# Performance work log

Measured on AMD Instinct MI355X. Metric: run time of the kernel, lower is better.

Reference implementation:

```python
import jax, jax.numpy as jnp
import numpy as np

B, S, I, H = 64, 1024, 256, 256

def setup_inputs() -> dict:
    key = jax.random.key(0)
    k1, k2, k3 = jax.random.split(key, 3)
    x = jax.random.normal(k1, (B, S, I), dtype=jnp.float32)
    W = jax.random.normal(k2, (4 * H, H + I), dtype=jnp.float32) * (1.0 / np.sqrt(H + I))
    b = jax.random.normal(k3, (4 * H,), dtype=jnp.float32) * 0.01
    return {"x": x, "W": W, "b": b}

def reference(x, W, b):
    batch, seq_len, input_size = x.shape
    hidden = W.shape[1] - input_size
    # torch concat order is (hidden, x): first H columns of W act on h, rest on x
    W_h = W[:, :hidden]          # [4H, H]
    W_x = W[:, hidden:]          # [4H, I]
    # precompute input projections for all timesteps: [B, S, 4H]
    x_proj = jnp.einsum('bsi,gi->bsg', x, W_x) + b

    h0 = jnp.zeros((batch, hidden), dtype=x.dtype)
    c0 = jnp.zeros((batch, hidden), dtype=x.dtype)

    def step(carry, xp_t):
        h, c = carry
        gates = h @ W_h.T + xp_t                     # [B, 4H]
        f, i, g, o = jnp.split(gates, 4, axis=1)     # chunk order: forget, input, convert, output
        f = jax.nn.sigmoid(f)
        i = jax.nn.sigmoid(i)
        g = jnp.tanh(g)
        o = jax.nn.sigmoid(o)
        c_new = f * c + i * g
        h_new = o * jnp.tanh(c_new)
        return (h_new, c_new), h_new

    (h_fin, c_fin), outs = jax.lax.scan(step, (h0, c0), jnp.swapaxes(x_proj, 0, 1))
    outputs = jnp.swapaxes(outs, 0, 1)               # [B, S, H]
    return outputs, (h_fin, c_fin)
```

## Files before the change

### kernel.cpp

```cpp
#include <hip/hip_runtime.h>

typedef __attribute__((ext_vector_type(8))) short short8;
typedef __attribute__((ext_vector_type(4))) float f32x4;
typedef __attribute__((ext_vector_type(4))) unsigned u32x4;

__device__ __forceinline__ unsigned short f2bf(float f) {
  unsigned int u = __float_as_uint(f);
  u = (u + 0x7fffu + ((u >> 16) & 1u)) >> 16;
  return (unsigned short)u;
}

__device__ __forceinline__ void xp_store(float* p, float v) { *p = v; }
__device__ __forceinline__ void xp_store(unsigned short* p, float v) { *p = f2bf(v); }
__device__ __forceinline__ float xp_ld(const float* p) { return *p; }
__device__ __forceinline__ float xp_ld(const unsigned short* p) {
  return __uint_as_float(((unsigned int)*p) << 16);
}

__device__ __forceinline__ float quad_sum(float a) {
  float t1 = __int_as_float(
      __builtin_amdgcn_update_dpp(0, __float_as_int(a), 177, 0xf, 0xf, true));
  a += t1;
  float t2 = __int_as_float(
      __builtin_amdgcn_update_dpp(0, __float_as_int(a), 78, 0xf, 0xf, true));
  return a + t2;
}

__global__ void prep_wx(const float* __restrict__ W, unsigned int* __restrict__ Wx2) {
  int i = blockIdx.x * 256 + threadIdx.x;
  int g = i >> 7, kk = i & 127;
  float lo = W[(size_t)g * 512 + 256 + 2 * kk];
  float hi = W[(size_t)g * 512 + 256 + 2 * kk + 1];
  Wx2[i] = (unsigned int)f2bf(lo) | ((unsigned int)f2bf(hi) << 16);
}

__global__ void prep_wh(const float* __restrict__ W, unsigned int* __restrict__ Wh2) {
  int i = blockIdx.x * 256 + threadIdx.x;
  int r = i >> 7, kk = i & 127;
  float lo = W[(size_t)r * 512 + 2 * kk];
  float hi = W[(size_t)r * 512 + 2 * kk + 1];
  Wh2[i] = (unsigned int)f2bf(lo) | ((unsigned int)f2bf(hi) << 16);
}

template <typename XPT>
__global__ __launch_bounds__(256, 4) void gemm_xp(const float* __restrict__ x,
                                                  const unsigned int* __restrict__ Wx2,
                                                  const float* __restrict__ bias,
                                                  XPT* __restrict__ xp) {
  __shared__ unsigned short As[128][40];
  __shared__ unsigned short Bs[128][40];
  const int m0 = blockIdx.y * 128, n0 = blockIdx.x * 128;
  const int tid = threadIdx.x, lane = tid & 63, w = tid >> 6;
  const int wr = w >> 1, wc = w & 1;
  const int r16 = lane & 15, kq = lane >> 4;
  f32x4 acc[4][4];
#pragma unroll
  for (int m = 0; m < 4; m++)
#pragma unroll
    for (int n = 0; n < 4; n++)
#pragma unroll
      for (int j = 0; j < 4; j++) acc[m][n][j] = 0.f;

  for (int kb = 0; kb < 256; kb += 32) {
    __syncthreads();
#pragma unroll
    for (int i = 0; i < 4; i++) {
      int idx = tid + i * 256;
      int row = idx >> 3, c4 = idx & 7;
      float4 v = *(const float4*)(x + (size_t)(m0 + row) * 256 + kb + c4 * 4);
      ushort4 s;
      s.x = f2bf(v.x); s.y = f2bf(v.y); s.z = f2bf(v.z); s.w = f2bf(v.w);
      *(ushort4*)&As[row][c4 * 4] = s;
    }
#pragma unroll
    for (int i = 0; i < 2; i++) {
      int idx = tid + i * 256;
      int row = idx >> 2, c = idx & 3;
      uint4 v = *(const uint4*)(Wx2 + (size_t)(n0 + row) * 128 + (kb >> 1) + c * 4);
      *(uint4*)&Bs[row][c * 8] = v;
    }
    __syncthreads();
    short8 a[4], bb[4];
#pragma unroll
    for (int m = 0; m < 4; m++)
      a[m] = *(const short8*)&As[wr * 64 + m * 16 + r16][kq * 8];
#pragma unroll
    for (int n = 0; n < 4; n++)
      bb[n] = *(const short8*)&Bs[wc * 64 + n * 16 + r16][kq * 8];
#pragma unroll
    for (int m = 0; m < 4; m++)
#pragma unroll
      for (int n = 0; n < 4; n++)
        acc[m][n] = __builtin_amdgcn_mfma_f32_16x16x32_bf16(a[m], bb[n], acc[m][n], 0, 0, 0);
  }
#pragma unroll
  for (int n = 0; n < 4; n++) {
    int gn = n0 + wc * 64 + n * 16 + r16;
    float bi = bias[gn];
#pragma unroll
    for (int m = 0; m < 4; m++) {
      int gm = m0 + wr * 64 + m * 16 + kq * 4;
#pragma unroll
      for (int j = 0; j < 4; j++) {
        xp_store(&xp[(size_t)(gm + j) * 1024 + gn], acc[m][n][j] + bi);
      }
    }
  }
}

template <typename XPT>
__global__ __attribute__((amdgpu_flat_work_group_size(512, 512),
                          amdgpu_waves_per_eu(2, 2)))
void lstm_rec(const unsigned* __restrict__ Wh2,
              const XPT* __restrict__ xp,
              float* __restrict__ out) {
  __shared__ u32x4 wot[16 * 512];
  __shared__ unsigned hsh[2][4][136];

  const int tid = threadIdx.x;
  const int b = blockIdx.x;
  const int v = tid >> 2, p = tid & 3;
  const int brow0 = b << 10;

  const unsigned* fA_p = Wh2 + (size_t)(v) * 128 + (p << 5);
  const unsigned* iA_p = Wh2 + (size_t)(256 + v) * 128 + (p << 5);
  const unsigned* gA_p = Wh2 + (size_t)(512 + v) * 128 + (p << 5);
  const unsigned* oA_p = Wh2 + (size_t)(768 + v) * 128 + (p << 5);
  const unsigned* fB_p = Wh2 + (size_t)(128 + v) * 128 + (p << 5);
  const unsigned* iB_p = Wh2 + (size_t)(384 + v) * 128 + (p << 5);
  const unsigned* gB_p = Wh2 + (size_t)(640 + v) * 128 + (p << 5);
  const unsigned* oB_p = Wh2 + (size_t)(896 + v) * 128 + (p << 5);
  u32x4 fA0, fA1, fA2, fA3, fA4, fA5, fA6, fA7;
  u32x4 iA0, iA1, iA2, iA3, iA4, iA5, iA6, iA7;
  u32x4 gA0, gA1, gA2, gA3, gA4, gA5, gA6, gA7;
  u32x4 fB0, fB1, fB2, fB3, fB4, fB5, fB6, fB7;
  u32x4 iB0, iB1, iB2, iB3, iB4, iB5, iB6, iB7;
  u32x4 gB0, gB1, gB2, gB3, gB4, gB5, gB6, gB7;
#define LOADROW8(P, R0, R1, R2, R3, R4, R5, R6, R7)                   \
  asm volatile("global_load_dwordx4 %0, %8, off\n\t"                  \
               "global_load_dwordx4 %1, %8, off offset:16\n\t"        \
               "global_load_dwordx4 %2, %8, off offset:32\n\t"        \
               "global_load_dwordx4 %3, %8, off offset:48\n\t"        \
               "global_load_dwordx4 %4, %8, off offset:64\n\t"        \
               "global_load_dwordx4 %5, %8, off offset:80\n\t"        \
               "global_load_dwordx4 %6, %8, off offset:96\n\t"        \
               "global_load_dwordx4 %7, %8, off offset:112"           \
               : "=&v"(R0), "=&v"(R1), "=&v"(R2), "=&v"(R3),          \
                 "=&v"(R4), "=&v"(R5), "=&v"(R6), "=&v"(R7)           \
               : "v"(P)                                               \
               : "memory")
  LOADROW8(fA_p, fA0, fA1, fA2, fA3, fA4, fA5, fA6, fA7);
  LOADROW8(iA_p, iA0, iA1, iA2, iA3, iA4, iA5, iA6, iA7);
  LOADROW8(gA_p, gA0, gA1, gA2, gA3, gA4, gA5, gA6, gA7);
  LOADROW8(fB_p, fB0, fB1, fB2, fB3, fB4, fB5, fB6, fB7);
  LOADROW8(iB_p, iB0, iB1, iB2, iB3, iB4, iB5, iB6, iB7);
  LOADROW8(gB_p, gB0, gB1, gB2, gB3, gB4, gB5, gB6, gB7);
#undef LOADROW8
  asm volatile("s_waitcnt vmcnt(0)" ::: "memory");

#pragma unroll
  for (int E = 0; E < 8; E++) {
    wot[(E << 9) + tid] = *(const u32x4*)(oA_p + (E << 2));
    wot[((E + 8) << 9) + tid] = *(const u32x4*)(oB_p + (E << 2));
  }

  for (int i = tid; i < 2 * 4 * 136; i += 512) ((unsigned*)hsh)[i] = 0u;
  float c0 = 0.f, c1 = 0.f;
  float* outp = out + ((size_t)brow0 << 8);
  __syncthreads();

#define BAR() asm volatile("s_waitcnt lgkmcnt(0)\n\ts_barrier" ::: "memory")
#define DOT2(ACC, WD, HD) \
  asm("v_dot2_f32_bf16 %0, %1, %2, %0" : "+v"(ACC) : "v"(WD), "v"(HD))
#define DOTC(FA, IA, GA, FB, IB, GB, OA, OB, HJ)                    \
  {                                                                 \
    DOT2(aF0, FA[0], (HJ)[0]); DOT2(aF0, FA[1], (HJ)[1]);           \
    DOT2(aF0, FA[2], (HJ)[2]); DOT2(aF0, FA[3], (HJ)[3]);           \
    DOT2(aI0, IA[0], (HJ)[0]); DOT2(aI0, IA[1], (HJ)[1]);           \
    DOT2(aI0, IA[2], (HJ)[2]); DOT2(aI0, IA[3], (HJ)[3]);           \
    DOT2(aG0, GA[0], (HJ)[0]); DOT2(aG0, GA[1], (HJ)[1]);           \
    DOT2(aG0, GA[2], (HJ)[2]); DOT2(aG0, GA[3], (HJ)[3]);           \
    DOT2(aO0, (OA)[0], (HJ)[0]); DOT2(aO0, (OA)[1], (HJ)[1]);       \
    DOT2(aO0, (OA)[2], (HJ)[2]); DOT2(aO0, (OA)[3], (HJ)[3]);       \
    DOT2(aF1, FB[0], (HJ)[0]); DOT2(aF1, FB[1], (HJ)[1]);           \
    DOT2(aF1, FB[2], (HJ)[2]); DOT2(aF1, FB[3], (HJ)[3]);           \
    DOT2(aI1, IB[0], (HJ)[0]); DOT2(aI1, IB[1], (HJ)[1]);           \
    DOT2(aI1, IB[2], (HJ)[2]); DOT2(aI1, IB[3], (HJ)[3]);           \
    DOT2(aG1, GB[0], (HJ)[0]); DOT2(aG1, GB[1], (HJ)[1]);           \
    DOT2(aG1, GB[2], (HJ)[2]); DOT2(aG1, GB[3], (HJ)[3]);           \
    DOT2(aO1, (OB)[0], (HJ)[0]); DOT2(aO1, (OB)[1], (HJ)[1]);       \
    DOT2(aO1, (OB)[2], (HJ)[2]); DOT2(aO1, (OB)[3], (HJ)[3]);       \
  }
#define HJC(HRX, J) (*(const u32x4*)&hsh[HRX][p][(p << 5) + ((J) << 2)])

#define LSTM1(AF, AI, AG, AO, X0, X1, X2, X3, CC, HOUT)             \
  {                                                                 \
    float gf = AF + X0, gi = AI + X1, gg = AG + X2, go = AO + X3;   \
    float f = 1.f / (1.f + __expf(-gf));                            \
    float ii = 1.f / (1.f + __expf(-gi));                           \
    float eg = __expf(2.f * gg);                                    \
    float gtv = (eg - 1.f) / (eg + 1.f);                            \
    float o = 1.f / (1.f + __expf(-go));                            \
    CC = f * CC + ii * gtv;                                         \
    float ec = __expf(2.f * CC);                                    \
    float tc = (ec - 1.f) / (ec + 1.f);                             \
    HOUT = o * tc;                                                  \
  }

#define STEP(T, HR, HW)                                                                \
  {                                                                                    \
    const int t = (T);                                                                 \
          \
    const XPT* xr = xp + ((size_t)(brow0 + t) << 10);                                  \
    float xv0 = xp_ld(xr + v),        xv1 = xp_ld(xr + 256 + v);                       \
    float xv2 = xp_ld(xr + 512 + v),  xv3 = xp_ld(xr + 768 + v);                       \
    float xw0 = xp_ld(xr + 128 + v),  xw1 = xp_ld(xr + 384 + v);                       \
    float xw2 = xp_ld(xr + 640 + v),  xw3 = xp_ld(xr + 896 + v);                       \
                                                     \
    u32x4 hX = HJC(HR, 0), oAX = wot[(0 << 9) + tid], oBX = wot[(8 << 9) + tid];       \
    u32x4 hY = HJC(HR, 1), oAY = wot[(1 << 9) + tid], oBY = wot[(9 << 9) + tid];       \
    float aF0 = 0.f, aI0 = 0.f, aG0 = 0.f, aO0 = 0.f;                                  \
    float aF1 = 0.f, aI1 = 0.f, aG1 = 0.f, aO1 = 0.f;                                  \
    DOTC(fA0, iA0, gA0, fB0, iB0, gB0, oAX, oBX, hX)                                   \
    hX = HJC(HR, 2); oAX = wot[(2 << 9) + tid]; oBX = wot[(10 << 9) + tid];            \
    DOTC(fA1, iA1, gA1, fB1, iB1, gB1, oAY, oBY, hY)                                   \
    hY = HJC(HR, 3); oAY = wot[(3 << 9) + tid]; oBY = wot[(11 << 9) + tid];            \
    DOTC(fA2, iA2, gA2, fB2, iB2, gB2, oAX, oBX, hX)                                   \
    hX = HJC(HR, 4); oAX = wot[(4 << 9) + tid]; oBX = wot[(12 << 9) + tid];            \
    DOTC(fA3, iA3, gA3, fB3, iB3, gB3, oAY, oBY, hY)                                   \
    hY = HJC(HR, 5); oAY = wot[(5 << 9) + tid]; oBY = wot[(13 << 9) + tid];            \
    DOTC(fA4, iA4, gA4, fB4, iB4, gB4, oAX, oBX, hX)                                   \
    hX = HJC(HR, 6); oAX = wot[(6 << 9) + tid]; oBX = wot[(14 << 9) + tid];            \
    DOTC(fA5, iA5, gA5, fB5, iB5, gB5, oAY, oBY, hY)                                   \
    hY = HJC(HR, 7); oAY = wot[(7 << 9) + tid]; oBY = wot[(15 << 9) + tid];            \
    DOTC(fA6, iA6, gA6, fB6, iB6, gB6, oAX, oBX, hX)                                   \
    DOTC(fA7, iA7, gA7, fB7, iB7, gB7, oAY, oBY, hY)                                   \
                 \
    aF0 = quad_sum(aF0); aI0 = quad_sum(aI0); aG0 = quad_sum(aG0); aO0 = quad_sum(aO0);\
    aF1 = quad_sum(aF1); aI1 = quad_sum(aI1); aG1 = quad_sum(aG1); aO1 = quad_sum(aO1);\
    float h0v, h1v;                                                                    \
    LSTM1(aF0, aI0, aG0, aO0, xv0, xv1, xv2, xv3, c0, h0v)                             \
    LSTM1(aF1, aI1, aG1, aO1, xw0, xw1, xw2, xw3, c1, h1v)                             \
                   \
    ((unsigned short*)&hsh[HW][p][0])[v] = f2bf(h0v);                                  \
    ((unsigned short*)&hsh[HW][p][0])[v + 128] = f2bf(h1v);                            \
    if (p == 0) {                                                                      \
      __builtin_nontemporal_store(h0v, outp + ((size_t)t << 8) + v);                   \
      __builtin_nontemporal_store(h1v, outp + ((size_t)t << 8) + v + 128);             \
      if (t == 1023) {                                                                 \
        out[16777216 + b * 256 + v] = h0v;                                             \
        out[16777216 + b * 256 + v + 128] = h1v;                                       \
        out[16777216 + 16384 + b * 256 + v] = c0;                                      \
        out[16777216 + 16384 + b * 256 + v + 128] = c1;                                \
      }                                                                                \
    }                                                                                  \
           \
    BAR();                                                                             \
  }

  for (int t2 = 0; t2 < 1024; t2 += 2) {
    STEP(t2, 1, 0)
    STEP(t2 + 1, 0, 1)
  }
#undef STEP
#undef LSTM1
#undef HJC
#undef DOTC
#undef DOT2
#undef BAR
}

extern "C" void kernel_launch(void* const* d_in, const int* in_sizes, int n_in,
                              void* d_out, int out_size, void* d_ws, size_t ws_size,
                              hipStream_t stream) {
  (void)in_sizes; (void)n_in; (void)out_size;
  const float* x = (const float*)d_in[0];
  const float* W = (const float*)d_in[1];
  const float* bias = (const float*)d_in[2];
  float* out = (float*)d_out;
  char* ws = (char*)d_ws;

  unsigned int* Wx2 = (unsigned int*)ws;
  unsigned int* Wh2 = (unsigned int*)(ws + 524288);
  char* xpmem = ws + 1048576;

  const size_t need32 = 1048576 + (size_t)65536 * 1024 * 4;

  prep_wx<<<512, 256, 0, stream>>>(W, Wx2);
  prep_wh<<<512, 256, 0, stream>>>(W, Wh2);

  if (ws_size >= need32) {
    gemm_xp<float><<<dim3(8, 512), 256, 0, stream>>>(x, Wx2, bias, (float*)xpmem);
    lstm_rec<float><<<64, 512, 0, stream>>>(Wh2, (const float*)xpmem, out);
  } else {
    gemm_xp<unsigned short><<<dim3(8, 512), 256, 0, stream>>>(x, Wx2, bias,
                                                              (unsigned short*)xpmem);
    lstm_rec<unsigned short><<<64, 512, 0, stream>>>(Wh2, (const unsigned short*)xpmem, out);
  }
}
```

Baseline: 2.106 ms.

## Replace dot2 recurrent matvec with MFMA 16x16x32 bf16 using prepacked fragment layout

The per-step recurrent h@W_h^T product switches from v_dot2_f32_bf16 plus quad DPP reductions to MFMA 16x16x32 bf16 instructions. W_h is repacked into MFMA B-fragment order by a new prep kernel and mostly held in registers, with the remaining k-tiles in LDS. The hidden state is broadcast as the A operand, so only the first row of each 16-row MFMA tile is useful and most of that MFMA work is wasted. The aim is to shorten the per-step critical path and drop the cross-lane reductions, at the cost of MFMA latency and fewer lanes doing the gate math and stores.

```diff
diff --git a/kernel.cpp b/kernel.cpp
--- a/kernel.cpp
+++ b/kernel.cpp
@@ -15,15 +15,6 @@
 __device__ __forceinline__ float xp_ld(const float* p) { return *p; }
 __device__ __forceinline__ float xp_ld(const unsigned short* p) {
   return __uint_as_float(((unsigned int)*p) << 16);
-}
-
-__device__ __forceinline__ float quad_sum(float a) {
-  float t1 = __int_as_float(
-      __builtin_amdgcn_update_dpp(0, __float_as_int(a), 177, 0xf, 0xf, true));
-  a += t1;
-  float t2 = __int_as_float(
-      __builtin_amdgcn_update_dpp(0, __float_as_int(a), 78, 0xf, 0xf, true));
-  return a + t2;
 }
 
 __global__ void prep_wx(const float* __restrict__ W, unsigned int* __restrict__ Wx2) {
@@ -34,12 +25,15 @@
   Wx2[i] = (unsigned int)f2bf(lo) | ((unsigned int)f2bf(hi) << 16);
 }
 
-__global__ void prep_wh(const float* __restrict__ W, unsigned int* __restrict__ Wh2) {
+__global__ void prep_whB(const float* __restrict__ W, unsigned* __restrict__ WhB) {
   int i = blockIdx.x * 256 + threadIdx.x;
-  int r = i >> 7, kk = i & 127;
-  float lo = W[(size_t)r * 512 + 2 * kk];
-  float hi = W[(size_t)r * 512 + 2 * kk + 1];
-  Wh2[i] = (unsigned int)f2bf(lo) | ((unsigned int)f2bf(hi) << 16);
+  int f = i >> 8, lane = (i >> 2) & 63, jd = i & 3;
+  int w = f >> 6, n = (f >> 3) & 7, kt = f & 7;
+  int g = 256 * (n >> 1) + 32 * w + 16 * (n & 1) + (lane & 15);
+  int k = kt * 32 + ((lane >> 4) << 3) + 2 * jd;
+  float lo = W[(size_t)g * 512 + k];
+  float hi = W[(size_t)g * 512 + k + 1];
+  WhB[i] = (unsigned)f2bf(lo) | ((unsigned)f2bf(hi) << 16);
 }
 
 template <typename XPT>
@@ -111,88 +105,66 @@
 template <typename XPT>
 __global__ __attribute__((amdgpu_flat_work_group_size(512, 512),
                           amdgpu_waves_per_eu(2, 2)))
-void lstm_rec(const unsigned* __restrict__ Wh2,
+void lstm_rec(const unsigned* __restrict__ WhB,
               const XPT* __restrict__ xp,
               float* __restrict__ out) {
-  __shared__ u32x4 wot[16 * 512];
-  __shared__ unsigned hsh[2][4][136];
+  __shared__ u32x4 wotB[16 * 512];
+  __shared__ unsigned short hl[2][256];
 
   const int tid = threadIdx.x;
   const int b = blockIdx.x;
-  const int v = tid >> 2, p = tid & 3;
+  const int lane = tid & 63, w = tid >> 6;
+  const int c = lane & 15;
   const int brow0 = b << 10;
 
-  const unsigned* fA_p = Wh2 + (size_t)(v) * 128 + (p << 5);
-  const unsigned* iA_p = Wh2 + (size_t)(256 + v) * 128 + (p << 5);
-  const unsigned* gA_p = Wh2 + (size_t)(512 + v) * 128 + (p << 5);
-  const unsigned* oA_p = Wh2 + (size_t)(768 + v) * 128 + (p << 5);
-  const unsigned* fB_p = Wh2 + (size_t)(128 + v) * 128 + (p << 5);
-  const unsigned* iB_p = Wh2 + (size_t)(384 + v) * 128 + (p << 5);
-  const unsigned* gB_p = Wh2 + (size_t)(640 + v) * 128 + (p << 5);
-  const unsigned* oB_p = Wh2 + (size_t)(896 + v) * 128 + (p << 5);
-  u32x4 fA0, fA1, fA2, fA3, fA4, fA5, fA6, fA7;
-  u32x4 iA0, iA1, iA2, iA3, iA4, iA5, iA6, iA7;
-  u32x4 gA0, gA1, gA2, gA3, gA4, gA5, gA6, gA7;
-  u32x4 fB0, fB1, fB2, fB3, fB4, fB5, fB6, fB7;
-  u32x4 iB0, iB1, iB2, iB3, iB4, iB5, iB6, iB7;
-  u32x4 gB0, gB1, gB2, gB3, gB4, gB5, gB6, gB7;
-#define LOADROW8(P, R0, R1, R2, R3, R4, R5, R6, R7)                   \
-  asm volatile("global_load_dwordx4 %0, %8, off\n\t"                  \
-               "global_load_dwordx4 %1, %8, off offset:16\n\t"        \
-               "global_load_dwordx4 %2, %8, off offset:32\n\t"        \
-               "global_load_dwordx4 %3, %8, off offset:48\n\t"        \
-               "global_load_dwordx4 %4, %8, off offset:64\n\t"        \
-               "global_load_dwordx4 %5, %8, off offset:80\n\t"        \
-               "global_load_dwordx4 %6, %8, off offset:96\n\t"        \
-               "global_load_dwordx4 %7, %8, off offset:112"           \
-               : "=&v"(R0), "=&v"(R1), "=&v"(R2), "=&v"(R3),          \
-                 "=&v"(R4), "=&v"(R5), "=&v"(R6), "=&v"(R7)           \
-               : "v"(P)                                               \
-               : "memory")
-  LOADROW8(fA_p, fA0, fA1, fA2, fA3, fA4, fA5, fA6, fA7);
-  LOADROW8(iA_p, iA0, iA1, iA2, iA3, iA4, iA5, iA6, iA7);
-  LOADROW8(gA_p, gA0, gA1, gA2, gA3, gA4, gA5, gA6, gA7);
-  LOADROW8(fB_p, fB0, fB1, fB2, fB3, fB4, fB5, fB6, fB7);
-  LOADROW8(iB_p, iB0, iB1, iB2, iB3, iB4, iB5, iB6, iB7);
-  LOADROW8(gB_p, gB0, gB1, gB2, gB3, gB4, gB5, gB6, gB7);
-#undef LOADROW8
+  short8 B00, B01, B02, B03, B04, B05, B10, B11, B12, B13, B14, B15;
+  short8 B20, B21, B22, B23, B24, B25, B30, B31, B32, B33, B34, B35;
+  short8 B40, B41, B42, B43, B44, B45, B50, B51, B52, B53, B54, B55;
+  short8 B60, B61, B62, B63, B64, B65, B70, B71, B72, B73, B74, B75;
+#define LOADB4(P, R0, R1, R2, R3)                                     \
+  asm volatile("global_load_dwordx4 %0, %4, off\n\t"                  \
+               "global_load_dwordx4 %1, %4, off offset:1024\n\t"      \
+               "global_load_dwordx4 %2, %4, off offset:2048\n\t"      \
+               "global_load_dwordx4 %3, %4, off offset:3072"          \
+               : "=&v"(R0), "=&v"(R1), "=&v"(R2), "=&v"(R3)           \
+               : "v"(P) : "memory")
+#define LOADB2(P, R0, R1)                                             \
+  asm volatile("global_load_dwordx4 %0, %2, off\n\t"                  \
+               "global_load_dwordx4 %1, %2, off offset:1024"          \
+               : "=&v"(R0), "=&v"(R1) : "v"(P) : "memory")
+#define LOADN(N, RA, RB, RC, RD, RE, RF)                              \
+  {                                                                   \
+    const unsigned* bp = WhB + ((((w << 3) + N) << 11)) + (lane << 2);\
+    LOADB4(bp, RA, RB, RC, RD);                                       \
+    LOADB2(bp + 1024, RE, RF);                                        \
+  }
+  LOADN(0, B00, B01, B02, B03, B04, B05)
+  LOADN(1, B10, B11, B12, B13, B14, B15)
+  LOADN(2, B20, B21, B22, B23, B24, B25)
+  LOADN(3, B30, B31, B32, B33, B34, B35)
+  LOADN(4, B40, B41, B42, B43, B44, B45)
+  LOADN(5, B50, B51, B52, B53, B54, B55)
+  LOADN(6, B60, B61, B62, B63, B64, B65)
+  LOADN(7, B70, B71, B72, B73, B74, B75)
+#undef LOADN
+#undef LOADB4
+#undef LOADB2
   asm volatile("s_waitcnt vmcnt(0)" ::: "memory");
 
 #pragma unroll
-  for (int E = 0; E < 8; E++) {
-    wot[(E << 9) + tid] = *(const u32x4*)(oA_p + (E << 2));
-    wot[((E + 8) << 9) + tid] = *(const u32x4*)(oB_p + (E << 2));
-  }
-
-  for (int i = tid; i < 2 * 4 * 136; i += 512) ((unsigned*)hsh)[i] = 0u;
+  for (int s = 0; s < 16; s++) {
+    int n = s >> 1, kt = 6 + (s & 1);
+    wotB[(s << 9) + tid] =
+        *(const u32x4*)(WhB + ((((w << 3) + n) << 3) + kt) * 256 + (lane << 2));
+  }
+
+  if (tid < 256) { hl[0][tid] = 0; hl[1][tid] = 0; }
   float c0 = 0.f, c1 = 0.f;
   float* outp = out + ((size_t)brow0 << 8);
   __syncthreads();
 
 #define BAR() asm volatile("s_waitcnt lgkmcnt(0)\n\ts_barrier" ::: "memory")
-#define DOT2(ACC, WD, HD) \
-  asm("v_dot2_f32_bf16 %0, %1, %2, %0" : "+v"(ACC) : "v"(WD), "v"(HD))
-#define DOTC(FA, IA, GA, FB, IB, GB, OA, OB, HJ)                    \
-  {                                                                 \
-    DOT2(aF0, FA[0], (HJ)[0]); DOT2(aF0, FA[1], (HJ)[1]);           \
-    DOT2(aF0, FA[2], (HJ)[2]); DOT2(aF0, FA[3], (HJ)[3]);           \
-    DOT2(aI0, IA[0], (HJ)[0]); DOT2(aI0, IA[1], (HJ)[1]);           \
-    DOT2(aI0, IA[2], (HJ)[2]); DOT2(aI0, IA[3], (HJ)[3]);           \
-    DOT2(aG0, GA[0], (HJ)[0]); DOT2(aG0, GA[1], (HJ)[1]);           \
-    DOT2(aG0, GA[2], (HJ)[2]); DOT2(aG0, GA[3], (HJ)[3]);           \
-    DOT2(aO0, (OA)[0], (HJ)[0]); DOT2(aO0, (OA)[1], (HJ)[1]);       \
-    DOT2(aO0, (OA)[2], (HJ)[2]); DOT2(aO0, (OA)[3], (HJ)[3]);       \
-    DOT2(aF1, FB[0], (HJ)[0]); DOT2(aF1, FB[1], (HJ)[1]);           \
-    DOT2(aF1, FB[2], (HJ)[2]); DOT2(aF1, FB[3], (HJ)[3]);           \
-    DOT2(aI1, IB[0], (HJ)[0]); DOT2(aI1, IB[1], (HJ)[1]);           \
-    DOT2(aI1, IB[2], (HJ)[2]); DOT2(aI1, IB[3], (HJ)[3]);           \
-    DOT2(aG1, GB[0], (HJ)[0]); DOT2(aG1, GB[1], (HJ)[1]);           \
-    DOT2(aG1, GB[2], (HJ)[2]); DOT2(aG1, GB[3], (HJ)[3]);           \
-    DOT2(aO1, (OB)[0], (HJ)[0]); DOT2(aO1, (OB)[1], (HJ)[1]);       \
-    DOT2(aO1, (OB)[2], (HJ)[2]); DOT2(aO1, (OB)[3], (HJ)[3]);       \
-  }
-#define HJC(HRX, J) (*(const u32x4*)&hsh[HRX][p][(p << 5) + ((J) << 2)])
-
+#define MF(A, Bf, C) __builtin_amdgcn_mfma_f32_16x16x32_bf16(A, Bf, C, 0, 0, 0)
 #define LSTM1(AF, AI, AG, AO, X0, X1, X2, X3, CC, HOUT)             \
   {                                                                 \
     float gf = AF + X0, gi = AI + X1, gg = AG + X2, go = AO + X3;   \
@@ -207,54 +179,79 @@
     HOUT = o * tc;                                                  \
   }
 
-#define STEP(T, HR, HW)                                                                \
+#define STEP(T, RS, WS)                                                                \
   {                                                                                    \
     const int t = (T);                                                                 \
-          \
+             \
     const XPT* xr = xp + ((size_t)(brow0 + t) << 10);                                  \
-    float xv0 = xp_ld(xr + v),        xv1 = xp_ld(xr + 256 + v);                       \
-    float xv2 = xp_ld(xr + 512 + v),  xv3 = xp_ld(xr + 768 + v);                       \
-    float xw0 = xp_ld(xr + 128 + v),  xw1 = xp_ld(xr + 384 + v);                       \
-    float xw2 = xp_ld(xr + 640 + v),  xw3 = xp_ld(xr + 896 + v);                       \
-                                                     \
-    u32x4 hX = HJC(HR, 0), oAX = wot[(0 << 9) + tid], oBX = wot[(8 << 9) + tid];       \
-    u32x4 hY = HJC(HR, 1), oAY = wot[(1 << 9) + tid], oBY = wot[(9 << 9) + tid];       \
-    float aF0 = 0.f, aI0 = 0.f, aG0 = 0.f, aO0 = 0.f;                                  \
-    float aF1 = 0.f, aI1 = 0.f, aG1 = 0.f, aO1 = 0.f;                                  \
-    DOTC(fA0, iA0, gA0, fB0, iB0, gB0, oAX, oBX, hX)                                   \
-    hX = HJC(HR, 2); oAX = wot[(2 << 9) + tid]; oBX = wot[(10 << 9) + tid];            \
-    DOTC(fA1, iA1, gA1, fB1, iB1, gB1, oAY, oBY, hY)                                   \
-    hY = HJC(HR, 3); oAY = wot[(3 << 9) + tid]; oBY = wot[(11 << 9) + tid];            \
-    DOTC(fA2, iA2, gA2, fB2, iB2, gB2, oAX, oBX, hX)                                   \
-    hX = HJC(HR, 4); oAX = wot[(4 << 9) + tid]; oBX = wot[(12 << 9) + tid];            \
-    DOTC(fA3, iA3, gA3, fB3, iB3, gB3, oAY, oBY, hY)                                   \
-    hY = HJC(HR, 5); oAY = wot[(5 << 9) + tid]; oBY = wot[(13 << 9) + tid];            \
-    DOTC(fA4, iA4, gA4, fB4, iB4, gB4, oAX, oBX, hX)                                   \
-    hX = HJC(HR, 6); oAX = wot[(6 << 9) + tid]; oBX = wot[(14 << 9) + tid];            \
-    DOTC(fA5, iA5, gA5, fB5, iB5, gB5, oAY, oBY, hY)                                   \
-    hY = HJC(HR, 7); oAY = wot[(7 << 9) + tid]; oBY = wot[(15 << 9) + tid];            \
-    DOTC(fA6, iA6, gA6, fB6, iB6, gB6, oAX, oBX, hX)                                   \
-    DOTC(fA7, iA7, gA7, fB7, iB7, gB7, oAY, oBY, hY)                                   \
-                 \
-    aF0 = quad_sum(aF0); aI0 = quad_sum(aI0); aG0 = quad_sum(aG0); aO0 = quad_sum(aO0);\
-    aF1 = quad_sum(aF1); aI1 = quad_sum(aI1); aG1 = quad_sum(aG1); aO1 = quad_sum(aO1);\
+    const int u0 = 32 * w + c;                                                         \
+    float xv0 = xp_ld(xr + u0),        xv1 = xp_ld(xr + u0 + 16);                      \
+    float xv2 = xp_ld(xr + 256 + u0),  xv3 = xp_ld(xr + 256 + u0 + 16);                \
+    float xv4 = xp_ld(xr + 512 + u0),  xv5 = xp_ld(xr + 512 + u0 + 16);                \
+    float xv6 = xp_ld(xr + 768 + u0),  xv7 = xp_ld(xr + 768 + u0 + 16);                \
+                            \
+    const short8* hfr = (const short8*)&hl[RS][0];                                     \
+    const int q = lane >> 4;                                                           \
+    const f32x4 Z = {0.f, 0.f, 0.f, 0.f};                                              \
+    short8 a = hfr[q];                                                                 \
+    f32x4 p0 = MF(a, B00, Z), p1 = MF(a, B10, Z), p2 = MF(a, B20, Z),                  \
+          p3 = MF(a, B30, Z), p4 = MF(a, B40, Z), p5 = MF(a, B50, Z),                  \
+          p6 = MF(a, B60, Z), p7 = MF(a, B70, Z);                                      \
+    a = hfr[4 + q];                                                                    \
+    p0 = MF(a, B01, p0); p1 = MF(a, B11, p1); p2 = MF(a, B21, p2);                     \
+    p3 = MF(a, B31, p3); p4 = MF(a, B41, p4); p5 = MF(a, B51, p5);                     \
+    p6 = MF(a, B61, p6); p7 = MF(a, B71, p7);                                          \
+    a = hfr[8 + q];                                                                    \
+    p0 = MF(a, B02, p0); p1 = MF(a, B12, p1); p2 = MF(a, B22, p2);                     \
+    p3 = MF(a, B32, p3); p4 = MF(a, B42, p4); p5 = MF(a, B52, p5);                     \
+    p6 = MF(a, B62, p6); p7 = MF(a, B72, p7);                                          \
+    a = hfr[12 + q];                                                                   \
+    p0 = MF(a, B03, p0); p1 = MF(a, B13, p1); p2 = MF(a, B23, p2);                     \
+    p3 = MF(a, B33, p3); p4 = MF(a, B43, p4); p5 = MF(a, B53, p5);                     \
+    p6 = MF(a, B63, p6); p7 = MF(a, B73, p7);                                          \
+    a = hfr[16 + q];                                                                   \
+    p0 = MF(a, B04, p0); p1 = MF(a, B14, p1); p2 = MF(a, B24, p2);                     \
+    p3 = MF(a, B34, p3); p4 = MF(a, B44, p4); p5 = MF(a, B54, p5);                     \
+    p6 = MF(a, B64, p6); p7 = MF(a, B74, p7);                                          \
+    a = hfr[20 + q];                                                                   \
+    p0 = MF(a, B05, p0); p1 = MF(a, B15, p1); p2 = MF(a, B25, p2);                     \
+    p3 = MF(a, B35, p3); p4 = MF(a, B45, p4); p5 = MF(a, B55, p5);                     \
+    p6 = MF(a, B65, p6); p7 = MF(a, B75, p7);                                          \
+                                                         \
+    a = hfr[24 + q];                                                                   \
+    p0 = MF(a, *(const short8*)&wotB[(0 << 9) + tid], p0);                             \
+    p1 = MF(a, *(const short8*)&wotB[(2 << 9) + tid], p1);                             \
+    p2 = MF(a, *(const short8*)&wotB[(4 << 9) + tid], p2);                             \
+    p3 = MF(a, *(const short8*)&wotB[(6 << 9) + tid], p3);                             \
+    p4 = MF(a, *(const short8*)&wotB[(8 << 9) + tid], p4);                             \
+    p5 = MF(a, *(const short8*)&wotB[(10 << 9) + tid], p5);                            \
+    p6 = MF(a, *(const short8*)&wotB[(12 << 9) + tid], p6);                            \
+    p7 = MF(a, *(const short8*)&wotB[(14 << 9) + tid], p7);                            \
+    a = hfr[28 + q];                                                                   \
+    p0 = MF(a, *(const short8*)&wotB[(1 << 9) + tid], p0);                             \
+    p1 = MF(a, *(const short8*)&wotB[(3 << 9) + tid], p1);                             \
+    p2 = MF(a, *(const short8*)&wotB[(5 << 9) + tid], p2);                             \
+    p3 = MF(a, *(const short8*)&wotB[(7 << 9) + tid], p3);                             \
+    p4 = MF(a, *(const short8*)&wotB[(9 << 9) + tid], p4);                             \
+    p5 = MF(a, *(const short8*)&wotB[(11 << 9) + tid], p5);                            \
+    p6 = MF(a, *(const short8*)&wotB[(13 << 9) + tid], p6);                            \
+    p7 = MF(a, *(const short8*)&wotB[(15 << 9) + tid], p7);                            \
+         \
     float h0v, h1v;                                                                    \
-    LSTM1(aF0, aI0, aG0, aO0, xv0, xv1, xv2, xv3, c0, h0v)                             \
-    LSTM1(aF1, aI1, aG1, aO1, xw0, xw1, xw2, xw3, c1, h1v)                             \
-                   \
-    ((unsigned short*)&hsh[HW][p][0])[v] = f2bf(h0v);                                  \
-    ((unsigned short*)&hsh[HW][p][0])[v + 128] = f2bf(h1v);                            \
-    if (p == 0) {                                                                      \
-      __builtin_nontemporal_store(h0v, outp + ((size_t)t << 8) + v);                   \
-      __builtin_nontemporal_store(h1v, outp + ((size_t)t << 8) + v + 128);             \
+    LSTM1(p0[0], p2[0], p4[0], p6[0], xv0, xv2, xv4, xv6, c0, h0v)                     \
+    LSTM1(p1[0], p3[0], p5[0], p7[0], xv1, xv3, xv5, xv7, c1, h1v)                     \
+    if (lane < 16) {                                                                   \
+      hl[WS][u0] = f2bf(h0v);                                                          \
+      hl[WS][u0 + 16] = f2bf(h1v);                                                     \
+      __builtin_nontemporal_store(h0v, outp + ((size_t)t << 8) + u0);                  \
+      __builtin_nontemporal_store(h1v, outp + ((size_t)t << 8) + u0 + 16);             \
       if (t == 1023) {                                                                 \
-        out[16777216 + b * 256 + v] = h0v;                                             \
-        out[16777216 + b * 256 + v + 128] = h1v;                                       \
-        out[16777216 + 16384 + b * 256 + v] = c0;                                      \
-        out[16777216 + 16384 + b * 256 + v + 128] = c1;                                \
+        out[16777216 + b * 256 + u0] = h0v;                                            \
+        out[16777216 + b * 256 + u0 + 16] = h1v;                                       \
+        out[16777216 + 16384 + b * 256 + u0] = c0;                                     \
+        out[16777216 + 16384 + b * 256 + u0 + 16] = c1;                                \
       }                                                                                \
     }                                                                                  \
-           \
     BAR();                                                                             \
   }
 
@@ -264,9 +261,7 @@
   }
 #undef STEP
 #undef LSTM1
-#undef HJC
-#undef DOTC
-#undef DOT2
+#undef MF
 #undef BAR
 }
 
@@ -281,20 +276,20 @@
   char* ws = (char*)d_ws;
 
   unsigned int* Wx2 = (unsigned int*)ws;
-  unsigned int* Wh2 = (unsigned int*)(ws + 524288);
+  unsigned int* WhB = (unsigned int*)(ws + 524288);
   char* xpmem = ws + 1048576;
 
   const size_t need32 = 1048576 + (size_t)65536 * 1024 * 4;
 
   prep_wx<<<512, 256, 0, stream>>>(W, Wx2);
-  prep_wh<<<512, 256, 0, stream>>>(W, Wh2);
+  prep_whB<<<512, 256, 0, stream>>>(W, WhB);
 
   if (ws_size >= need32) {
     gemm_xp<float><<<dim3(8, 512), 256, 0, stream>>>(x, Wx2, bias, (float*)xpmem);
-    lstm_rec<float><<<64, 512, 0, stream>>>(Wh2, (const float*)xpmem, out);
+    lstm_rec<float><<<64, 512, 0, stream>>>(WhB, (const float*)xpmem, out);
   } else {
     gemm_xp<unsigned short><<<dim3(8, 512), 256, 0, stream>>>(x, Wx2, bias,
                                                               (unsigned short*)xpmem);
-    lstm_rec<unsigned short><<<64, 512, 0, stream>>>(Wh2, (const unsigned short*)xpmem, out);
-  }
-}
+    lstm_rec<unsigned short><<<64, 512, 0, stream>>>(WhB, (const unsigned short*)xpmem, out);
+  }
+}
```

Result: slower. 2.780 ms (+32.0%).
